# Optimization experiments

Hardware: AMD Instinct MI355X
Metric: run time of the kernel (lower is better)

## Reference

```python
import jax, jax.numpy as jnp
import numpy as np

B, T, NEMBD, HEAD = 8, 2048, 1024, 64

def setup_inputs() -> dict:
    key = jax.random.key(0)
    ks = jax.random.split(key, 6)
    return {
        "values": jax.random.normal(ks[0], (B, T, NEMBD), dtype=jnp.float32),
        "keys": jax.random.normal(ks[1], (B, T, NEMBD), dtype=jnp.float32),
        "queries": jax.random.normal(ks[2], (B, T, NEMBD), dtype=jnp.float32),
        "Wk": jax.random.normal(ks[3], (NEMBD, HEAD), dtype=jnp.float32) * (NEMBD ** -0.5),
        "Wq": jax.random.normal(ks[4], (NEMBD, HEAD), dtype=jnp.float32) * (NEMBD ** -0.5),
        "Wv": jax.random.normal(ks[5], (NEMBD, HEAD), dtype=jnp.float32) * (NEMBD ** -0.5),
    }

def reference(values, keys, queries, Wk, Wq, Wv):
    Bq, Tq, C = queries.shape  # C = nEmbd; original scales by C**-0.5 (NOT headSize)
    k = keys @ Wk              # [B,T,H]
    q = queries @ Wq           # [B,T,H]
    v = values @ Wv            # [B,T,H]
    weight = jnp.einsum('bth,bsh->bts', q, k) * (C ** -0.5)  # [B,T,T]
    causal = jnp.tril(jnp.ones((Tq, Tq), dtype=bool))
    weight = jnp.where(causal, weight, -jnp.inf)
    weight = jax.nn.softmax(weight, axis=-1)
    # dropout = 0.0 (eval): identity
    out = jnp.einsum('bts,bsh->bth', weight, v)  # [B,T,H]
    return out
```

## Files before the change

kernel.cpp:

```cpp
#include <hip/hip_runtime.h>
#include <hip/hip_bf16.h>

typedef __bf16 bf16x8 __attribute__((ext_vector_type(8)));
typedef float f32x4 __attribute__((ext_vector_type(4)));
typedef unsigned short u16x8 __attribute__((ext_vector_type(8)));

#define NB 8
#define NT 2048
#define NC 1024
#define NH 64

__device__ __forceinline__ unsigned short bfbits(float f) {
    return __builtin_bit_cast(unsigned short, (__bf16)f);
}

__global__ __launch_bounds__(256) void wt_kernel(const float* __restrict__ Wq,
                                                 const float* __restrict__ Wk,
                                                 const float* __restrict__ Wv,
                                                 unsigned short* __restrict__ Wt) {
    int idx = blockIdx.x * 256 + threadIdx.x;
    int n = idx >> 16;
    int r = idx & 65535;
    int c = r >> 6;
    int h = r & 63;
    const float* W = (n == 0) ? Wq : ((n == 1) ? Wk : Wv);
    float x = W[c * 64 + h];
    Wt[(n << 16) + h * 1024 + c] = bfbits(x);
}

__global__ __launch_bounds__(256, 4) void proj_kernel(const float* __restrict__ Xv,
                                                      const float* __restrict__ Xk,
                                                      const float* __restrict__ Xq,
                                                      const unsigned short* __restrict__ Wt,
                                                      unsigned short* __restrict__ Q,
                                                      unsigned short* __restrict__ K,
                                                      unsigned short* __restrict__ VT) {
    __shared__ __align__(16) char Xs[64 * 256];
    __shared__ __align__(16) char Ws[64 * 256];

    int type = blockIdx.x >> 8;
    int mt   = blockIdx.x & 255;
    int row0 = mt << 6;
    const float* X = (type == 0) ? Xq : ((type == 1) ? Xk : Xv);
    const unsigned short* W = Wt + (type << 16);

    int tid  = threadIdx.x;
    int w    = tid >> 6;
    int lane = tid & 63;
    int lo = lane & 15, hi = lane >> 4;

    f32x4 acc[4];
#pragma unroll
    for (int ct = 0; ct < 4; ++ct) acc[ct] = 0.f;

    for (int kc = 0; kc < 8; ++kc) {
        f32x4 xr[8];
#pragma unroll
        for (int i = 0; i < 8; ++i) {
            int f4 = tid + 256 * i;
            int r  = f4 >> 5, c4 = f4 & 31;
            xr[i] = __builtin_nontemporal_load(
                (const f32x4*)(X + (size_t)(row0 + r) * NC + kc * 128 + c4 * 4));
        }
        u16x8 wr_[4];
#pragma unroll
        for (int i = 0; i < 4; ++i) {
            int s16 = tid + 256 * i;
            int h = s16 >> 4, sl = s16 & 15;
            wr_[i] = *(const u16x8*)(W + h * 1024 + kc * 128 + sl * 8);
        }
        __syncthreads();
#pragma unroll
        for (int i = 0; i < 8; ++i) {
            int f4 = tid + 256 * i;
            int r  = f4 >> 5, c4 = f4 & 31;
            ushort4 bv;
            bv.x = bfbits(xr[i][0]); bv.y = bfbits(xr[i][1]);
            bv.z = bfbits(xr[i][2]); bv.w = bfbits(xr[i][3]);
            int byte = r * 256 + ((c4 * 8) ^ ((r & 7) << 4));
            *(ushort4*)(Xs + byte) = bv;
        }
#pragma unroll
        for (int i = 0; i < 4; ++i) {
            int s16 = tid + 256 * i;
            int h = s16 >> 4, sl = s16 & 15;
            int byte = h * 256 + ((sl * 16) ^ ((h & 7) << 4));
            *(u16x8*)(Ws + byte) = wr_[i];
        }
        __syncthreads();
#pragma unroll
        for (int ks = 0; ks < 4; ++ks) {
            int coff = (ks * 64 + hi * 16) ^ ((lo & 7) << 4);
            bf16x8 af = *(const bf16x8*)(Xs + (w * 16 + lo) * 256 + coff);
#pragma unroll
            for (int ct = 0; ct < 4; ++ct) {
                bf16x8 bf = *(const bf16x8*)(Ws + (ct * 16 + lo) * 256 + coff);
                acc[ct] = __builtin_amdgcn_mfma_f32_16x16x32_bf16(af, bf, acc[ct], 0, 0, 0);
            }
        }
    }

    if (type < 2) {
        unsigned short* O = (type == 0) ? Q : K;
#pragma unroll
        for (int ct = 0; ct < 4; ++ct)
#pragma unroll
            for (int r = 0; r < 4; ++r) {
                int row = row0 + w * 16 + hi * 4 + r;
                int h = lo + 16 * ct;
                O[(size_t)row * NH + h] = bfbits(acc[ct][r]);
            }
    } else {
        int trow = row0 + w * 16 + hi * 4;
        int b = trow >> 11;
        int t = trow & 2047;
#pragma unroll
        for (int ct = 0; ct < 4; ++ct) {
            int h = lo + 16 * ct;
            ushort4 pk;
            pk.x = bfbits(acc[ct][0]);
            pk.y = bfbits(acc[ct][1]);
            pk.z = bfbits(acc[ct][2]);
            pk.w = bfbits(acc[ct][3]);
            *(ushort4*)(VT + (size_t)(b * NH + h) * NT + t) = pk;
        }
    }
}

__global__ __launch_bounds__(256) void attn_kernel(const unsigned short* __restrict__ Q,
                                                   const unsigned short* __restrict__ K,
                                                   const unsigned short* __restrict__ VT,
                                                   float* __restrict__ out) {
    __shared__ __align__(16) unsigned short p_lds[4 * 512];
    __shared__ __align__(16) float acc_lds[4 * 16 * 64];
    __shared__ float m_lds[4][16];
    __shared__ float l_lds[4][16];

    int b  = blockIdx.x & 7;
    int qt = blockIdx.x >> 3;
    int q0 = qt << 4;
    int w    = threadIdx.x >> 6;
    int lane = threadIdx.x & 63;
    int lo = lane & 15, hi = lane >> 4;

    const float SC = 0.03125f * 1.44269504088896340736f;
    const unsigned short* qb = Q + (size_t)(b * NT + q0 + lo) * NH + hi * 8;
    bf16x8 qr0 = *(const bf16x8*)(qb);
    bf16x8 qr1 = *(const bf16x8*)(qb + 32);
    bf16x8 qf0, qf1;
#pragma unroll
    for (int j = 0; j < 8; ++j) {
        qf0[j] = (__bf16)((float)qr0[j] * SC);
        qf1[j] = (__bf16)((float)qr1[j] * SC);
    }

    int Ctot = (q0 + 16 + 31) >> 5;
    int c0 = (Ctot * w) >> 2;
    int c1 = (Ctot * (w + 1)) >> 2;

    float m[4], l[4];
    f32x4 acc[4];
#pragma unroll
    for (int r = 0; r < 4; ++r) { m[r] = -1e30f; l[r] = 0.f; }
#pragma unroll
    for (int ct = 0; ct < 4; ++ct) acc[ct] = 0.f;

    unsigned short* pl = p_lds + w * 512;

    for (int c = c0; c < c1; ++c) {
        int s0 = c << 5;
        const unsigned short* kb = K + (size_t)(b * NT + s0 + lo) * NH + hi * 8;
        f32x4 S0 = 0.f, S1 = 0.f;
        S0 = __builtin_amdgcn_mfma_f32_16x16x32_bf16(qf0, *(const bf16x8*)(kb), S0, 0, 0, 0);
        S0 = __builtin_amdgcn_mfma_f32_16x16x32_bf16(qf1, *(const bf16x8*)(kb + 32), S0, 0, 0, 0);
        S1 = __builtin_amdgcn_mfma_f32_16x16x32_bf16(qf0, *(const bf16x8*)(kb + 16 * NH), S1, 0, 0, 0);
        S1 = __builtin_amdgcn_mfma_f32_16x16x32_bf16(qf1, *(const bf16x8*)(kb + 16 * NH + 32), S1, 0, 0, 0);

        int s_a = s0 + lo, s_b = s0 + 16 + lo;
        float z0[4], z1[4], mt_[4];
#pragma unroll
        for (int r = 0; r < 4; ++r) {
            int qi = q0 + hi * 4 + r;
            z0[r] = (s_a <= qi) ? S0[r] : -1e30f;
            z1[r] = (s_b <= qi) ? S1[r] : -1e30f;
            mt_[r] = fmaxf(z0[r], z1[r]);
        }
#pragma unroll
        for (int d = 1; d < 16; d <<= 1)
#pragma unroll
            for (int r = 0; r < 4; ++r)
                mt_[r] = fmaxf(mt_[r], __shfl_xor(mt_[r], d, 16));

        float p0[4], p1[4], rs[4];
#pragma unroll
        for (int r = 0; r < 4; ++r) {
            float mn = fmaxf(m[r], mt_[r]);
            float al = exp2f(m[r] - mn);
            int qi = q0 + hi * 4 + r;
            p0[r] = (s_a <= qi) ? exp2f(z0[r] - mn) : 0.f;
            p1[r] = (s_b <= qi) ? exp2f(z1[r] - mn) : 0.f;
            rs[r] = p0[r] + p1[r];
            m[r] = mn;
            l[r] *= al;
            acc[0][r] *= al; acc[1][r] *= al; acc[2][r] *= al; acc[3][r] *= al;
        }
#pragma unroll
        for (int d = 1; d < 16; d <<= 1)
#pragma unroll
            for (int r = 0; r < 4; ++r)
                rs[r] += __shfl_xor(rs[r], d, 16);
#pragma unroll
        for (int r = 0; r < 4; ++r) {
            l[r] += rs[r];
            int ql = hi * 4 + r;
            pl[ql * 32 + lo]      = bfbits(p0[r]);
            pl[ql * 32 + 16 + lo] = bfbits(p1[r]);
        }
        bf16x8 pa = *(const bf16x8*)(pl + lo * 32 + hi * 8);
        const unsigned short* vb = VT + (size_t)(b * NH + lo) * NT + s0 + hi * 8;
#pragma unroll
        for (int ct = 0; ct < 4; ++ct) {
            bf16x8 vv = *(const bf16x8*)(vb + ct * 16 * NT);
            acc[ct] = __builtin_amdgcn_mfma_f32_16x16x32_bf16(pa, vv, acc[ct], 0, 0, 0);
        }
    }

#pragma unroll
    for (int r = 0; r < 4; ++r) {
        int ql = hi * 4 + r;
#pragma unroll
        for (int ct = 0; ct < 4; ++ct)
            acc_lds[(w * 16 + ql) * 64 + lo + 16 * ct] = acc[ct][r];
    }
    if (lo == 0) {
#pragma unroll
        for (int r = 0; r < 4; ++r) {
            m_lds[w][hi * 4 + r] = m[r];
            l_lds[w][hi * 4 + r] = l[r];
        }
    }
    __syncthreads();

    int q  = threadIdx.x >> 4;
    int h0 = (threadIdx.x & 15) << 2;
    float M = fmaxf(fmaxf(m_lds[0][q], m_lds[1][q]), fmaxf(m_lds[2][q], m_lds[3][q]));
    float L = 0.f;
    float ox = 0.f, oy = 0.f, oz = 0.f, ow = 0.f;
#pragma unroll
    for (int ww = 0; ww < 4; ++ww) {
        float a_ = exp2f(m_lds[ww][q] - M);
        L += a_ * l_lds[ww][q];
        const float* p = acc_lds + (ww * 16 + q) * 64 + h0;
        ox += a_ * p[0]; oy += a_ * p[1]; oz += a_ * p[2]; ow += a_ * p[3];
    }
    float inv = 1.0f / L;
    float4 res = make_float4(ox * inv, oy * inv, oz * inv, ow * inv);
    *(float4*)(out + (size_t)(b * NT + q0 + q) * NH + h0) = res;
}

extern "C" void kernel_launch(void* const* d_in, const int* in_sizes, int n_in,
                              void* d_out, int out_size, void* d_ws, size_t ws_size,
                              hipStream_t stream) {
    const float* values  = (const float*)d_in[0];
    const float* keys    = (const float*)d_in[1];
    const float* queries = (const float*)d_in[2];
    const float* Wk = (const float*)d_in[3];
    const float* Wq = (const float*)d_in[4];
    const float* Wv = (const float*)d_in[5];
    float* out = (float*)d_out;

    unsigned short* Wt = (unsigned short*)d_ws;
    unsigned short* Qb = Wt + 196608;
    unsigned short* Kb = Qb + 1048576;
    unsigned short* VT = Kb + 1048576;

    wt_kernel<<<768, 256, 0, stream>>>(Wq, Wk, Wv, Wt);
    proj_kernel<<<768, 256, 0, stream>>>(values, keys, queries, Wt, Qb, Kb, VT);
    attn_kernel<<<1024, 256, 0, stream>>>(Qb, Kb, VT, out);
}
```

Measured before the change: 88.66 us.

## Pair causal query tiles per block and prefetch K/V tiles in attention

Each attention block now processes two query tiles, j and 127-j, so every block gets roughly equal causal work, and the grid is halved. Inside the key loop, the next K tile is loaded into registers ahead of use, and the V loads are issued before the softmax math to hide memory latency. This adds register pressure and an extra barrier per tile pair, and it reduces the number of resident blocks.

```diff
diff --git a/kernel.cpp b/kernel.cpp
--- a/kernel.cpp
+++ b/kernel.cpp
@@ -136,126 +136,148 @@
     __shared__ float m_lds[4][16];
     __shared__ float l_lds[4][16];
 
-    int b  = blockIdx.x & 7;
-    int qt = blockIdx.x >> 3;
-    int q0 = qt << 4;
+    int b = blockIdx.x & 7;
+    int j = blockIdx.x >> 3;
     int w    = threadIdx.x >> 6;
     int lane = threadIdx.x & 63;
     int lo = lane & 15, hi = lane >> 4;
 
     const float SC = 0.03125f * 1.44269504088896340736f;
-    const unsigned short* qb = Q + (size_t)(b * NT + q0 + lo) * NH + hi * 8;
-    bf16x8 qr0 = *(const bf16x8*)(qb);
-    bf16x8 qr1 = *(const bf16x8*)(qb + 32);
-    bf16x8 qf0, qf1;
-#pragma unroll
-    for (int j = 0; j < 8; ++j) {
-        qf0[j] = (__bf16)((float)qr0[j] * SC);
-        qf1[j] = (__bf16)((float)qr1[j] * SC);
+    unsigned short* pl = p_lds + w * 512;
+
+    for (int t2 = 0; t2 < 2; ++t2) {
+        int qt = t2 ? (127 - j) : j;
+        int q0 = qt << 4;
+
+        const unsigned short* qb = Q + (size_t)(b * NT + q0 + lo) * NH + hi * 8;
+        bf16x8 qr0 = *(const bf16x8*)(qb);
+        bf16x8 qr1 = *(const bf16x8*)(qb + 32);
+        bf16x8 qf0, qf1;
+#pragma unroll
+        for (int jj = 0; jj < 8; ++jj) {
+            qf0[jj] = (__bf16)((float)qr0[jj] * SC);
+            qf1[jj] = (__bf16)((float)qr1[jj] * SC);
+        }
+
+        int Ctot = (q0 + 47) >> 5;
+        int c0 = (Ctot * w) >> 2;
+        int c1 = (Ctot * (w + 1)) >> 2;
+
+        float m[4], l[4];
+        f32x4 acc[4];
+#pragma unroll
+        for (int r = 0; r < 4; ++r) { m[r] = -1e30f; l[r] = 0.f; }
+#pragma unroll
+        for (int ct = 0; ct < 4; ++ct) acc[ct] = 0.f;
+
+        const unsigned short* kp = K + (size_t)(b * NT + (c0 << 5) + lo) * NH + hi * 8;
+        bf16x8 kn0 = *(const bf16x8*)(kp);
+        bf16x8 kn1 = *(const bf16x8*)(kp + 32);
+        bf16x8 kn2 = *(const bf16x8*)(kp + 16 * NH);
+        bf16x8 kn3 = *(const bf16x8*)(kp + 16 * NH + 32);
+
+        for (int c = c0; c < c1; ++c) {
+            int s0 = c << 5;
+            bf16x8 k0 = kn0, k1 = kn1, k2 = kn2, k3 = kn3;
+            if (c + 1 < c1) {
+                const unsigned short* kp2 = K + (size_t)(b * NT + ((c + 1) << 5) + lo) * NH + hi * 8;
+                kn0 = *(const bf16x8*)(kp2);
+                kn1 = *(const bf16x8*)(kp2 + 32);
+                kn2 = *(const bf16x8*)(kp2 + 16 * NH);
+                kn3 = *(const bf16x8*)(kp2 + 16 * NH + 32);
+            }
+            f32x4 S0 = 0.f, S1 = 0.f;
+            S0 = __builtin_amdgcn_mfma_f32_16x16x32_bf16(qf0, k0, S0, 0, 0, 0);
+            S0 = __builtin_amdgcn_mfma_f32_16x16x32_bf16(qf1, k1, S0, 0, 0, 0);
+            S1 = __builtin_amdgcn_mfma_f32_16x16x32_bf16(qf0, k2, S1, 0, 0, 0);
+            S1 = __builtin_amdgcn_mfma_f32_16x16x32_bf16(qf1, k3, S1, 0, 0, 0);
+
+            const unsigned short* vb = VT + (size_t)(b * NH + lo) * NT + s0 + hi * 8;
+            bf16x8 vv0 = *(const bf16x8*)(vb);
+            bf16x8 vv1 = *(const bf16x8*)(vb + 16 * NT);
+            bf16x8 vv2 = *(const bf16x8*)(vb + 32 * NT);
+            bf16x8 vv3 = *(const bf16x8*)(vb + 48 * NT);
+
+            int s_a = s0 + lo, s_b = s0 + 16 + lo;
+            float z0[4], z1[4], mt_[4];
+#pragma unroll
+            for (int r = 0; r < 4; ++r) {
+                int qi = q0 + hi * 4 + r;
+                z0[r] = (s_a <= qi) ? S0[r] : -1e30f;
+                z1[r] = (s_b <= qi) ? S1[r] : -1e30f;
+                mt_[r] = fmaxf(z0[r], z1[r]);
+            }
+#pragma unroll
+            for (int d = 1; d < 16; d <<= 1)
+#pragma unroll
+                for (int r = 0; r < 4; ++r)
+                    mt_[r] = fmaxf(mt_[r], __shfl_xor(mt_[r], d, 16));
+
+            float p0[4], p1[4], rs[4];
+#pragma unroll
+            for (int r = 0; r < 4; ++r) {
+                float mn = fmaxf(m[r], mt_[r]);
+                float al = exp2f(m[r] - mn);
+                int qi = q0 + hi * 4 + r;
+                p0[r] = (s_a <= qi) ? exp2f(z0[r] - mn) : 0.f;
+                p1[r] = (s_b <= qi) ? exp2f(z1[r] - mn) : 0.f;
+                rs[r] = p0[r] + p1[r];
+                m[r] = mn;
+                l[r] *= al;
+                acc[0][r] *= al; acc[1][r] *= al; acc[2][r] *= al; acc[3][r] *= al;
+            }
+#pragma unroll
+            for (int d = 1; d < 16; d <<= 1)
+#pragma unroll
+                for (int r = 0; r < 4; ++r)
+                    rs[r] += __shfl_xor(rs[r], d, 16);
+#pragma unroll
+            for (int r = 0; r < 4; ++r) {
+                l[r] += rs[r];
+                int ql = hi * 4 + r;
+                pl[ql * 32 + lo]      = bfbits(p0[r]);
+                pl[ql * 32 + 16 + lo] = bfbits(p1[r]);
+            }
+            bf16x8 pa = *(const bf16x8*)(pl + lo * 32 + hi * 8);
+            acc[0] = __builtin_amdgcn_mfma_f32_16x16x32_bf16(pa, vv0, acc[0], 0, 0, 0);
+            acc[1] = __builtin_amdgcn_mfma_f32_16x16x32_bf16(pa, vv1, acc[1], 0, 0, 0);
+            acc[2] = __builtin_amdgcn_mfma_f32_16x16x32_bf16(pa, vv2, acc[2], 0, 0, 0);
+            acc[3] = __builtin_amdgcn_mfma_f32_16x16x32_bf16(pa, vv3, acc[3], 0, 0, 0);
+        }
+
+#pragma unroll
+        for (int r = 0; r < 4; ++r) {
+            int ql = hi * 4 + r;
+#pragma unroll
+            for (int ct = 0; ct < 4; ++ct)
+                acc_lds[(w * 16 + ql) * 64 + lo + 16 * ct] = acc[ct][r];
+        }
+        if (lo == 0) {
+#pragma unroll
+            for (int r = 0; r < 4; ++r) {
+                m_lds[w][hi * 4 + r] = m[r];
+                l_lds[w][hi * 4 + r] = l[r];
+            }
+        }
+        __syncthreads();
+
+        int q  = threadIdx.x >> 4;
+        int h0 = (threadIdx.x & 15) << 2;
+        float M = fmaxf(fmaxf(m_lds[0][q], m_lds[1][q]), fmaxf(m_lds[2][q], m_lds[3][q]));
+        float L = 0.f;
+        float ox = 0.f, oy = 0.f, oz = 0.f, ow = 0.f;
+#pragma unroll
+        for (int ww = 0; ww < 4; ++ww) {
+            float a_ = exp2f(m_lds[ww][q] - M);
+            L += a_ * l_lds[ww][q];
+            const float* p = acc_lds + (ww * 16 + q) * 64 + h0;
+            ox += a_ * p[0]; oy += a_ * p[1]; oz += a_ * p[2]; ow += a_ * p[3];
+        }
+        float inv = 1.0f / L;
+        float4 res = make_float4(ox * inv, oy * inv, oz * inv, ow * inv);
+        *(float4*)(out + (size_t)(b * NT + q0 + q) * NH + h0) = res;
+        __syncthreads();
     }
-
-    int Ctot = (q0 + 16 + 31) >> 5;
-    int c0 = (Ctot * w) >> 2;
-    int c1 = (Ctot * (w + 1)) >> 2;
-
-    float m[4], l[4];
-    f32x4 acc[4];
-#pragma unroll
-    for (int r = 0; r < 4; ++r) { m[r] = -1e30f; l[r] = 0.f; }
-#pragma unroll
-    for (int ct = 0; ct < 4; ++ct) acc[ct] = 0.f;
-
-    unsigned short* pl = p_lds + w * 512;
-
-    for (int c = c0; c < c1; ++c) {
-        int s0 = c << 5;
-        const unsigned short* kb = K + (size_t)(b * NT + s0 + lo) * NH + hi * 8;
-        f32x4 S0 = 0.f, S1 = 0.f;
-        S0 = __builtin_amdgcn_mfma_f32_16x16x32_bf16(qf0, *(const bf16x8*)(kb), S0, 0, 0, 0);
-        S0 = __builtin_amdgcn_mfma_f32_16x16x32_bf16(qf1, *(const bf16x8*)(kb + 32), S0, 0, 0, 0);
-        S1 = __builtin_amdgcn_mfma_f32_16x16x32_bf16(qf0, *(const bf16x8*)(kb + 16 * NH), S1, 0, 0, 0);
-        S1 = __builtin_amdgcn_mfma_f32_16x16x32_bf16(qf1, *(const bf16x8*)(kb + 16 * NH + 32), S1, 0, 0, 0);
-
-        int s_a = s0 + lo, s_b = s0 + 16 + lo;
-        float z0[4], z1[4], mt_[4];
-#pragma unroll
-        for (int r = 0; r < 4; ++r) {
-            int qi = q0 + hi * 4 + r;
-            z0[r] = (s_a <= qi) ? S0[r] : -1e30f;
-            z1[r] = (s_b <= qi) ? S1[r] : -1e30f;
-            mt_[r] = fmaxf(z0[r], z1[r]);
-        }
-#pragma unroll
-        for (int d = 1; d < 16; d <<= 1)
-#pragma unroll
-            for (int r = 0; r < 4; ++r)
-                mt_[r] = fmaxf(mt_[r], __shfl_xor(mt_[r], d, 16));
-
-        float p0[4], p1[4], rs[4];
-#pragma unroll
-        for (int r = 0; r < 4; ++r) {
-            float mn = fmaxf(m[r], mt_[r]);
-            float al = exp2f(m[r] - mn);
-            int qi = q0 + hi * 4 + r;
-            p0[r] = (s_a <= qi) ? exp2f(z0[r] - mn) : 0.f;
-            p1[r] = (s_b <= qi) ? exp2f(z1[r] - mn) : 0.f;
-            rs[r] = p0[r] + p1[r];
-            m[r] = mn;
-            l[r] *= al;
-            acc[0][r] *= al; acc[1][r] *= al; acc[2][r] *= al; acc[3][r] *= al;
-        }
-#pragma unroll
-        for (int d = 1; d < 16; d <<= 1)
-#pragma unroll
-            for (int r = 0; r < 4; ++r)
-                rs[r] += __shfl_xor(rs[r], d, 16);
-#pragma unroll
-        for (int r = 0; r < 4; ++r) {
-            l[r] += rs[r];
-            int ql = hi * 4 + r;
-            pl[ql * 32 + lo]      = bfbits(p0[r]);
-            pl[ql * 32 + 16 + lo] = bfbits(p1[r]);
-        }
-        bf16x8 pa = *(const bf16x8*)(pl + lo * 32 + hi * 8);
-        const unsigned short* vb = VT + (size_t)(b * NH + lo) * NT + s0 + hi * 8;
-#pragma unroll
-        for (int ct = 0; ct < 4; ++ct) {
-            bf16x8 vv = *(const bf16x8*)(vb + ct * 16 * NT);
-            acc[ct] = __builtin_amdgcn_mfma_f32_16x16x32_bf16(pa, vv, acc[ct], 0, 0, 0);
-        }
-    }
-
-#pragma unroll
-    for (int r = 0; r < 4; ++r) {
-        int ql = hi * 4 + r;
-#pragma unroll
-        for (int ct = 0; ct < 4; ++ct)
-            acc_lds[(w * 16 + ql) * 64 + lo + 16 * ct] = acc[ct][r];
-    }
-    if (lo == 0) {
-#pragma unroll
-        for (int r = 0; r < 4; ++r) {
-            m_lds[w][hi * 4 + r] = m[r];
-            l_lds[w][hi * 4 + r] = l[r];
-        }
-    }
-    __syncthreads();
-
-    int q  = threadIdx.x >> 4;
-    int h0 = (threadIdx.x & 15) << 2;
-    float M = fmaxf(fmaxf(m_lds[0][q], m_lds[1][q]), fmaxf(m_lds[2][q], m_lds[3][q]));
-    float L = 0.f;
-    float ox = 0.f, oy = 0.f, oz = 0.f, ow = 0.f;
-#pragma unroll
-    for (int ww = 0; ww < 4; ++ww) {
-        float a_ = exp2f(m_lds[ww][q] - M);
-        L += a_ * l_lds[ww][q];
-        const float* p = acc_lds + (ww * 16 + q) * 64 + h0;
-        ox += a_ * p[0]; oy += a_ * p[1]; oz += a_ * p[2]; ow += a_ * p[3];
-    }
-    float inv = 1.0f / L;
-    float4 res = make_float4(ox * inv, oy * inv, oz * inv, ow * inv);
-    *(float4*)(out + (size_t)(b * NT + q0 + q) * NH + h0) = res;
 }
 
 extern "C" void kernel_launch(void* const* d_in, const int* in_sizes, int n_in,
@@ -276,5 +298,5 @@
 
     wt_kernel<<<768, 256, 0, stream>>>(Wq, Wk, Wv, Wt);
     proj_kernel<<<768, 256, 0, stream>>>(values, keys, queries, Wt, Qb, Kb, VT);
-    attn_kernel<<<1024, 256, 0, stream>>>(Qb, Kb, VT, out);
-}
+    attn_kernel<<<512, 256, 0, stream>>>(Qb, Kb, VT, out);
+}
```

Result: faster. 82.59 us (-6.8%).
